# Performance work log

Measured on AMD Instinct MI355X. Metric: run time of the kernel, lower is better.

## Reference

```python
import jax, jax.numpy as jnp
import numpy as np

BINS = 10
EPS_BIN = 0.0001  # matches torch floor(g * (bins - 0.0001))
MIN_GD = 0.0001


def setup_inputs() -> dict:
    key = jax.random.key(0)
    k1, k2, k3 = jax.random.split(key, 3)
    N, C = 1048576, 64
    x = jax.random.normal(k1, (N, C), dtype=jnp.float32)
    target = jax.random.randint(k2, (N,), 0, C, dtype=jnp.int32)
    weight = jax.random.uniform(k3, (C,), dtype=jnp.float32)
    return {"x": x, "target": target, "weight": weight, "stage": 2}


def reference(x, target, weight, stage):
    # log-softmax over classes, gather log p_t per sample
    log_p = jax.nn.log_softmax(x, axis=-1)                       # [N, C]
    log_pt = jnp.take_along_axis(log_p, target[:, None], axis=1)[:, 0]  # [N]

    # NLL (reduction='none'); stage 2 applies per-class weights
    if stage == 1:
        ce = -log_pt
    else:
        ce = -weight[target] * log_pt

    # gradient magnitude g = |pt - 1|, detached (histogram is non-differentiable)
    g = jax.lax.stop_gradient(jnp.abs(jnp.exp(log_pt) - 1.0))
    bin_idx = jnp.floor(g * (BINS - EPS_BIN)).astype(jnp.int32)   # [N] in [0, BINS)

    # histogram via scatter-add (first call: _last_bin_count is None, no EMA)
    bin_count = jnp.zeros((BINS,), dtype=x.dtype).at[bin_idx].add(1.0)
    nonempty = jnp.sum(bin_count > 0).astype(x.dtype)
    gd = jnp.clip(bin_count * nonempty, MIN_GD, None)
    beta = 1.0 / gd

    # gather beta per sample and reweight; reduction='mean'
    loss = jnp.mean(beta[bin_idx] * ce)
    return loss
```

## Files before the change

### kernel.cpp

```cpp
#include <hip/hip_runtime.h>
#include <cmath>


#define BINS 10
#define MAIN_BLOCKS 2048
#define STRIDE 66

__global__ __launch_bounds__(64) void ghmc_main_kernel(
    const float* __restrict__ x,
    const int* __restrict__ target,
    const float* __restrict__ weight,
    const int* __restrict__ stage_p,
    double* __restrict__ part_ce,
    unsigned int* __restrict__ part_cnt,
    int N)
{
    __shared__ float        s_x[64 * STRIDE];
    __shared__ double       s_ce[BINS];
    __shared__ unsigned int s_cnt[BINS];

    const int tid = threadIdx.x;
    if (tid < BINS) { s_ce[tid] = 0.0; s_cnt[tid] = 0u; }

    const int stage = *stage_p;
    const float4* __restrict__ x4 = (const float4*)x;
    const unsigned int ntiles = (unsigned int)N >> 6;

    unsigned int cnt9 = 0;
    double ce9 = 0.0;

    for (unsigned int tile = blockIdx.x; tile < ntiles; tile += MAIN_BLOCKS) {
        const size_t tb4 = (size_t)tile << 10;

        #pragma unroll
        for (int j = 0; j < 16; j++) {
            int i = (j << 6) + tid;
            float4 vv = x4[tb4 + (unsigned)i];
            int r = i >> 4, c = (i & 15) << 2;
            float* p = &s_x[r * STRIDE + c];
            ((float2*)p)[0]       = make_float2(vv.x, vv.y);
            ((float2*)(p + 2))[0] = make_float2(vv.z, vv.w);
        }

        const float2* __restrict__ vp = (const float2*)&s_x[tid * STRIDE];
        float2 v2[32];
        #pragma unroll
        for (int e = 0; e < 32; e++) v2[e] = vp[e];

        float mx[32];
        #pragma unroll
        for (int e = 0; e < 32; e++) mx[e] = fmaxf(v2[e].x, v2[e].y);
        #pragma unroll
        for (int w = 16; w > 0; w >>= 1) {
            #pragma unroll
            for (int e = 0; e < w; e++) mx[e] = fmaxf(mx[e], mx[e + w]);
        }
        const float m = mx[0];

        float sm[32];
        #pragma unroll
        for (int e = 0; e < 32; e++)
            sm[e] = expf(v2[e].x - m) + expf(v2[e].y - m);
        #pragma unroll
        for (int w = 16; w > 0; w >>= 1) {
            #pragma unroll
            for (int e = 0; e < w; e++) sm[e] += sm[e + w];
        }
        const float s = sm[0];

        int   t  = target[(size_t)tile * 64 + (unsigned)tid];
        float vt = s_x[tid * STRIDE + t];
        float log_pt = (vt - m) - logf(s);
        float w  = (stage == 1) ? 1.0f : weight[t];
        float ce = -(w * log_pt);
        float g  = fabsf(expf(log_pt) - 1.0f);
        int b = (int)floorf(g * 9.9999f);
        b = b < 0 ? 0 : (b > 9 ? 9 : b);
        if (b == 9) {
            cnt9++;
            ce9 += (double)ce;
        } else {
            atomicAdd(&s_cnt[b], 1u);
            atomicAdd(&s_ce[b], (double)ce);
        }
    }

    #pragma unroll
    for (int off = 32; off > 0; off >>= 1) {
        cnt9 += __shfl_xor(cnt9, off, 64);
        ce9  += __shfl_xor(ce9, off, 64);
    }
    if (tid == 0) { s_cnt[9] += cnt9; s_ce[9] += ce9; }

    if (tid < BINS) {
        part_ce [tid * MAIN_BLOCKS + blockIdx.x] = s_ce[tid];
        part_cnt[tid * MAIN_BLOCKS + blockIdx.x] = s_cnt[tid];
    }
}

__global__ __launch_bounds__(1024) void ghmc_final_kernel(
    const double* __restrict__ part_ce,
    const unsigned int* __restrict__ part_cnt,
    float* __restrict__ out, int N)
{
    __shared__ double       s_ce[BINS];
    __shared__ unsigned int s_cnt[BINS];
    if (threadIdx.x < BINS) { s_ce[threadIdx.x] = 0.0; s_cnt[threadIdx.x] = 0u; }
    __syncthreads();

    #pragma unroll
    for (int b = 0; b < BINS; b++) {
        double ce = 0.0; unsigned int cnt = 0u;
        for (int k = threadIdx.x; k < MAIN_BLOCKS; k += 1024) {
            ce  += part_ce [b * MAIN_BLOCKS + k];
            cnt += part_cnt[b * MAIN_BLOCKS + k];
        }
        #pragma unroll
        for (int off = 32; off > 0; off >>= 1) {
            ce  += __shfl_xor(ce, off, 64);
            cnt += __shfl_xor(cnt, off, 64);
        }
        if ((threadIdx.x & 63) == 0) {
            atomicAdd(&s_ce[b], ce);
            atomicAdd(&s_cnt[b], cnt);
        }
    }
    __syncthreads();

    if (threadIdx.x == 0) {
        int nonempty = 0;
        #pragma unroll
        for (int b = 0; b < BINS; b++) nonempty += (s_cnt[b] > 0u) ? 1 : 0;
        double total = 0.0;
        #pragma unroll
        for (int b = 0; b < BINS; b++) {
            float gd = (float)s_cnt[b] * (float)nonempty;
            gd = fmaxf(gd, 1e-4f);
            total += s_ce[b] / (double)gd;
        }
        out[0] = (float)(total / (double)N);
    }
}

extern "C" void kernel_launch(void* const* d_in, const int* in_sizes, int n_in,
                              void* d_out, int out_size, void* d_ws, size_t ws_size,
                              hipStream_t stream) {
    const float* x       = (const float*)d_in[0];
    const int* target    = (const int*)d_in[1];
    const float* weight  = (const float*)d_in[2];
    const int* stage_p   = (const int*)d_in[3];
    const int N = in_sizes[1];

    double* part_ce = (double*)d_ws;
    unsigned int* part_cnt = (unsigned int*)(part_ce + BINS * MAIN_BLOCKS);

    ghmc_main_kernel<<<MAIN_BLOCKS, 64, 0, stream>>>(x, target, weight, stage_p,
                                                     part_ce, part_cnt, N);
    ghmc_final_kernel<<<1, 1024, 0, stream>>>(part_ce, part_cnt, (float*)d_out, N);
}
```

Measured before the change: 377.9 us.

## Process rows with 16-lane groups and DPP reductions instead of LDS transpose

Each wavefront now handles four rows per step, with sixteen lanes each loading one float4 of a row. Max and sum reductions use DPP cross-lane ops, so the shared-memory transpose and per-thread 64-element loops are gone. The kernel also moves to 256-thread blocks and prefetches the next quad of rows in registers. Only one lane per row does the bin math, which adds divergence, and the shared bins see more atomic contention with four waves per block.

```diff
diff --git a/kernel.cpp b/kernel.cpp
--- a/kernel.cpp
+++ b/kernel.cpp
@@ -4,9 +4,19 @@
 
 #define BINS 10
 #define MAIN_BLOCKS 2048
-#define STRIDE 66
 
-__global__ __launch_bounds__(64) void ghmc_main_kernel(
+template <int CTRL>
+__device__ __forceinline__ float dpp_f(float x) {
+    int r = __builtin_amdgcn_update_dpp(0, __builtin_bit_cast(int, x),
+                                        CTRL, 0xF, 0xF, true);
+    return __builtin_bit_cast(float, r);
+}
+#define DPP_XOR1 0xB1
+#define DPP_XOR2 0x4E
+#define DPP_ROR4 0x124
+#define DPP_ROR8 0x128
+
+__global__ __launch_bounds__(256) void ghmc_main_kernel(
     const float* __restrict__ x,
     const int* __restrict__ target,
     const float* __restrict__ weight,
@@ -15,73 +25,73 @@
     unsigned int* __restrict__ part_cnt,
     int N)
 {
-    __shared__ float        s_x[64 * STRIDE];
     __shared__ double       s_ce[BINS];
     __shared__ unsigned int s_cnt[BINS];
 
     const int tid = threadIdx.x;
     if (tid < BINS) { s_ce[tid] = 0.0; s_cnt[tid] = 0u; }
+    __syncthreads();
 
     const int stage = *stage_p;
     const float4* __restrict__ x4 = (const float4*)x;
-    const unsigned int ntiles = (unsigned int)N >> 6;
+    const unsigned nquads = (unsigned)N >> 2;
+    const unsigned lane   = (unsigned)tid & 63u;
+    const unsigned sub    = lane >> 4;
+    const unsigned quad   = lane & 15u;
+    const unsigned gw     = blockIdx.x * 4u + ((unsigned)tid >> 6);
+    const unsigned NW     = MAIN_BLOCKS * 4u;
 
-    unsigned int cnt9 = 0;
-    double ce9 = 0.0;
+    unsigned cnt9 = 0;
+    double   ce9  = 0.0;
 
-    for (unsigned int tile = blockIdx.x; tile < ntiles; tile += MAIN_BLOCKS) {
-        const size_t tb4 = (size_t)tile << 10;
+    unsigned q = gw;
+    if (q < nquads) {
+        float4 v = x4[(size_t)q * 64 + lane];
+        int    t = target[q * 4u + sub];
+        for (;;) {
+            const unsigned qn = q + NW;
+            const bool more = qn < nquads;
+            float4 vn; int tn;
+            if (more) {
+                vn = x4[(size_t)qn * 64 + lane];
+                tn = target[qn * 4u + sub];
+            }
 
-        #pragma unroll
-        for (int j = 0; j < 16; j++) {
-            int i = (j << 6) + tid;
-            float4 vv = x4[tb4 + (unsigned)i];
-            int r = i >> 4, c = (i & 15) << 2;
-            float* p = &s_x[r * STRIDE + c];
-            ((float2*)p)[0]       = make_float2(vv.x, vv.y);
-            ((float2*)(p + 2))[0] = make_float2(vv.z, vv.w);
-        }
+            float m = fmaxf(fmaxf(v.x, v.y), fmaxf(v.z, v.w));
+            m = fmaxf(m, dpp_f<DPP_XOR1>(m));
+            m = fmaxf(m, dpp_f<DPP_XOR2>(m));
+            m = fmaxf(m, dpp_f<DPP_ROR4>(m));
+            m = fmaxf(m, dpp_f<DPP_ROR8>(m));
 
-        const float2* __restrict__ vp = (const float2*)&s_x[tid * STRIDE];
-        float2 v2[32];
-        #pragma unroll
-        for (int e = 0; e < 32; e++) v2[e] = vp[e];
+            float e0 = expf(v.x - m), e1 = expf(v.y - m);
+            float e2 = expf(v.z - m), e3 = expf(v.w - m);
+            float s = (e0 + e1) + (e2 + e3);
+            s += dpp_f<DPP_ROR4>(s);
+            s += dpp_f<DPP_ROR8>(s);
+            s += dpp_f<DPP_XOR1>(s);
+            s += dpp_f<DPP_XOR2>(s);
 
-        float mx[32];
-        #pragma unroll
-        for (int e = 0; e < 32; e++) mx[e] = fmaxf(v2[e].x, v2[e].y);
-        #pragma unroll
-        for (int w = 16; w > 0; w >>= 1) {
-            #pragma unroll
-            for (int e = 0; e < w; e++) mx[e] = fmaxf(mx[e], mx[e + w]);
-        }
-        const float m = mx[0];
+            if (quad == (unsigned)(t >> 2)) {
+                const int c = t & 3;
+                float vt = (c & 1) ? ((c & 2) ? v.w : v.y)
+                                   : ((c & 2) ? v.z : v.x);
+                float log_pt = (vt - m) - logf(s);
+                float w  = (stage == 1) ? 1.0f : weight[t];
+                float ce = -(w * log_pt);
+                float g  = fabsf(expf(log_pt) - 1.0f);
+                int b = (int)floorf(g * 9.9999f);
+                b = b < 0 ? 0 : (b > 9 ? 9 : b);
+                if (b == 9) {
+                    cnt9++;
+                    ce9 += (double)ce;
+                } else {
+                    atomicAdd(&s_cnt[b], 1u);
+                    atomicAdd(&s_ce[b], (double)ce);
+                }
+            }
 
-        float sm[32];
-        #pragma unroll
-        for (int e = 0; e < 32; e++)
-            sm[e] = expf(v2[e].x - m) + expf(v2[e].y - m);
-        #pragma unroll
-        for (int w = 16; w > 0; w >>= 1) {
-            #pragma unroll
-            for (int e = 0; e < w; e++) sm[e] += sm[e + w];
-        }
-        const float s = sm[0];
-
-        int   t  = target[(size_t)tile * 64 + (unsigned)tid];
-        float vt = s_x[tid * STRIDE + t];
-        float log_pt = (vt - m) - logf(s);
-        float w  = (stage == 1) ? 1.0f : weight[t];
-        float ce = -(w * log_pt);
-        float g  = fabsf(expf(log_pt) - 1.0f);
-        int b = (int)floorf(g * 9.9999f);
-        b = b < 0 ? 0 : (b > 9 ? 9 : b);
-        if (b == 9) {
-            cnt9++;
-            ce9 += (double)ce;
-        } else {
-            atomicAdd(&s_cnt[b], 1u);
-            atomicAdd(&s_ce[b], (double)ce);
+            if (!more) break;
+            v = vn; t = tn; q = qn;
         }
     }
 
@@ -90,7 +100,11 @@
         cnt9 += __shfl_xor(cnt9, off, 64);
         ce9  += __shfl_xor(ce9, off, 64);
     }
-    if (tid == 0) { s_cnt[9] += cnt9; s_ce[9] += ce9; }
+    if (lane == 0) {
+        atomicAdd(&s_cnt[9], cnt9);
+        atomicAdd(&s_ce[9], ce9);
+    }
+    __syncthreads();
 
     if (tid < BINS) {
         part_ce [tid * MAIN_BLOCKS + blockIdx.x] = s_ce[tid];
@@ -154,7 +168,7 @@
     double* part_ce = (double*)d_ws;
     unsigned int* part_cnt = (unsigned int*)(part_ce + BINS * MAIN_BLOCKS);
 
-    ghmc_main_kernel<<<MAIN_BLOCKS, 64, 0, stream>>>(x, target, weight, stage_p,
-                                                     part_ce, part_cnt, N);
+    ghmc_main_kernel<<<MAIN_BLOCKS, 256, 0, stream>>>(x, target, weight, stage_p,
+                                                      part_ce, part_cnt, N);
     ghmc_final_kernel<<<1, 1024, 0, stream>>>(part_ce, part_cnt, (float*)d_out, N);
 }
```

Result: no change. 371.3 us (-1.7%).
